# Performance work log

Measured on AMD Instinct MI355X. Metric: run time of the kernel, lower is better.

## Reference

```python
import jax, jax.numpy as jnp
import numpy as np


def setup_inputs() -> dict:
    key = jax.random.key(0)
    x = jax.random.normal(key, (256, 128, 2048), dtype=jnp.float32)
    return {"x": x}


def reference(x) -> jnp.ndarray:
    # x: (batch, channels, time)
    # 1) average reference: subtract mean across channels per (batch, time)
    x = x - jnp.mean(x, axis=1, keepdims=True)
    # 2) channel-wise zscore: mean/std over time axis per (batch, channel)
    mean = jnp.mean(x, axis=2, keepdims=True)
    std = jnp.std(x, axis=2, keepdims=True)  # population std (ddof=0), matches np.std
    std = jnp.where(std == 0, jnp.ones_like(std), std)
    return (x - mean) / std
```

## Files before the change

kernel.cpp:

```cpp
#include <hip/hip_runtime.h>


#define B 256
#define C 128
#define T 2048
#define T4 (T / 4)

typedef float f4 __attribute__((ext_vector_type(4)));

__launch_bounds__(1024)
__global__ void eeg_fused(const float* __restrict__ x, float* __restrict__ out) {
    const int b = blockIdx.x;
    const int tid = threadIdx.x;

    __shared__ float4 mu4[T4];
    __shared__ float4 part[T4];

    const float4* __restrict__ xb =
        reinterpret_cast<const float4*>(x) + (size_t)b * C * T4;
    float4* __restrict__ ob =
        reinterpret_cast<float4*>(out) + (size_t)b * C * T4;

    {
        const int t4 = tid & (T4 - 1);
        const int g  = tid >> 9;
        const float4* __restrict__ xp = xb + (size_t)(g * 64) * T4 + t4;

        float4 acc = make_float4(0.f, 0.f, 0.f, 0.f);
        #pragma unroll 8
        for (int k = 0; k < 64; ++k) {
            float4 v = xp[(size_t)k * T4];
            acc.x += v.x; acc.y += v.y; acc.z += v.z; acc.w += v.w;
        }
        if (g) part[t4] = acc;
        else   mu4[t4]  = acc;
        __syncthreads();
        if (!g) {
            const float invC = 1.0f / (float)C;
            float4 p = part[t4];
            float4 m = mu4[t4];
            m.x = (m.x + p.x) * invC;
            m.y = (m.y + p.y) * invC;
            m.z = (m.z + p.z) * invC;
            m.w = (m.w + p.w) * invC;
            mu4[t4] = m;
        }
        __syncthreads();
    }

    const int wave = tid >> 6;
    const int lane = tid & 63;
    const float invT = 1.0f / (float)T;

    for (int cc = wave; cc < C; cc += 16) {
        const int c = (C - 1) - cc;
        const float4* __restrict__ xc = xb + (size_t)c * T4;

        float4 y[8];
        float sum = 0.f, sq = 0.f;
        #pragma unroll
        for (int j = 0; j < 8; ++j) {
            float4 v = xc[lane + j * 64];
            float4 m = mu4[lane + j * 64];
            y[j].x = v.x - m.x; y[j].y = v.y - m.y;
            y[j].z = v.z - m.z; y[j].w = v.w - m.w;
            sum += (y[j].x + y[j].y) + (y[j].z + y[j].w);
            sq  += (y[j].x * y[j].x + y[j].y * y[j].y)
                 + (y[j].z * y[j].z + y[j].w * y[j].w);
        }

        #pragma unroll
        for (int off = 32; off > 0; off >>= 1) {
            sum += __shfl_xor(sum, off, 64);
            sq  += __shfl_xor(sq,  off, 64);
        }

        float mean = sum * invT;
        float var  = fmaxf(sq * invT - mean * mean, 0.f);
        float sd   = sqrtf(var);
        float inv  = (sd == 0.f) ? 1.0f : 1.0f / sd;

        float4* __restrict__ oc = ob + (size_t)c * T4;
        #pragma unroll
        for (int j = 0; j < 8; ++j) {
            f4 o = { (y[j].x - mean) * inv,
                     (y[j].y - mean) * inv,
                     (y[j].z - mean) * inv,
                     (y[j].w - mean) * inv };
            __builtin_nontemporal_store(
                o, reinterpret_cast<f4*>(oc + lane + j * 64));
        }
    }
}

extern "C" void kernel_launch(void* const* d_in, const int* in_sizes, int n_in,
                              void* d_out, int out_size, void* d_ws, size_t ws_size,
                              hipStream_t stream) {
    const float* x = (const float*)d_in[0];
    float* out = (float*)d_out;
    (void)d_ws; (void)ws_size;

    eeg_fused<<<B, 1024, 0, stream>>>(x, out);
}
```

Before: 465.8 us.

## Split fused kernel into channel-mean pass and per-row zscore kernel

Replaces the single per-batch 1024-thread kernel with two launches: one computing the channel mean per (batch,time) into workspace using many small blocks, and one where each wave z-scores a single (batch,channel) row. This raises parallelism far beyond one block per batch and removes the intra-block barrier phase. The cost is a second full read of the input from global memory plus a workspace round-trip and an extra launch.

```diff
diff --git a/kernel.cpp b/kernel.cpp
--- a/kernel.cpp
+++ b/kernel.cpp
@@ -8,88 +8,86 @@
 
 typedef float f4 __attribute__((ext_vector_type(4)));
 
-__launch_bounds__(1024)
-__global__ void eeg_fused(const float* __restrict__ x, float* __restrict__ out) {
-    const int b = blockIdx.x;
+__launch_bounds__(256)
+__global__ void mu_kernel(const float* __restrict__ x, float* __restrict__ mu) {
+    const int b = blockIdx.y;
+    const int t0 = blockIdx.x * 256;
     const int tid = threadIdx.x;
+    const int wave = tid >> 6;
+    const int lane = tid & 63;
 
-    __shared__ float4 mu4[T4];
-    __shared__ float4 part[T4];
+    const float4* __restrict__ xp =
+        reinterpret_cast<const float4*>(x + ((size_t)b * C + wave * 32) * T + t0);
 
-    const float4* __restrict__ xb =
-        reinterpret_cast<const float4*>(x) + (size_t)b * C * T4;
-    float4* __restrict__ ob =
-        reinterpret_cast<float4*>(out) + (size_t)b * C * T4;
-
-    {
-        const int t4 = tid & (T4 - 1);
-        const int g  = tid >> 9;
-        const float4* __restrict__ xp = xb + (size_t)(g * 64) * T4 + t4;
-
-        float4 acc = make_float4(0.f, 0.f, 0.f, 0.f);
-        #pragma unroll 8
-        for (int k = 0; k < 64; ++k) {
-            float4 v = xp[(size_t)k * T4];
-            acc.x += v.x; acc.y += v.y; acc.z += v.z; acc.w += v.w;
-        }
-        if (g) part[t4] = acc;
-        else   mu4[t4]  = acc;
-        __syncthreads();
-        if (!g) {
-            const float invC = 1.0f / (float)C;
-            float4 p = part[t4];
-            float4 m = mu4[t4];
-            m.x = (m.x + p.x) * invC;
-            m.y = (m.y + p.y) * invC;
-            m.z = (m.z + p.z) * invC;
-            m.w = (m.w + p.w) * invC;
-            mu4[t4] = m;
-        }
-        __syncthreads();
+    float4 acc = make_float4(0.f, 0.f, 0.f, 0.f);
+    #pragma unroll 8
+    for (int k = 0; k < 32; ++k) {
+        float4 v = xp[(size_t)k * T4 + lane];
+        acc.x += v.x; acc.y += v.y; acc.z += v.z; acc.w += v.w;
     }
 
-    const int wave = tid >> 6;
-    const int lane = tid & 63;
+    __shared__ float4 part[4][64];
+    part[wave][lane] = acc;
+    __syncthreads();
+
+    if (wave == 0) {
+        float4 p0 = part[0][lane], p1 = part[1][lane];
+        float4 p2 = part[2][lane], p3 = part[3][lane];
+        const float invC = 1.0f / (float)C;
+        float4 s;
+        s.x = (p0.x + p1.x + p2.x + p3.x) * invC;
+        s.y = (p0.y + p1.y + p2.y + p3.y) * invC;
+        s.z = (p0.z + p1.z + p2.z + p3.z) * invC;
+        s.w = (p0.w + p1.w + p2.w + p3.w) * invC;
+        reinterpret_cast<float4*>(mu + (size_t)b * T + t0)[lane] = s;
+    }
+}
+
+__launch_bounds__(256)
+__global__ void zscore_wave(const float* __restrict__ x,
+                            const float* __restrict__ mu,
+                            float* __restrict__ out) {
+    const int wave = threadIdx.x >> 6;
+    const int lane = threadIdx.x & 63;
+    const int bc = blockIdx.x * 4 + wave;
+    const int b = bc >> 7;
+
+    const float4* __restrict__ xc = reinterpret_cast<const float4*>(x) + (size_t)bc * T4;
+    const float4* __restrict__ mc = reinterpret_cast<const float4*>(mu) + (size_t)b * T4;
+
+    float4 y[8];
+    float sum = 0.f, sq = 0.f;
+    #pragma unroll
+    for (int j = 0; j < 8; ++j) {
+        float4 v = xc[lane + j * 64];
+        float4 m = mc[lane + j * 64];
+        y[j].x = v.x - m.x; y[j].y = v.y - m.y;
+        y[j].z = v.z - m.z; y[j].w = v.w - m.w;
+        sum += (y[j].x + y[j].y) + (y[j].z + y[j].w);
+        sq  += (y[j].x * y[j].x + y[j].y * y[j].y)
+             + (y[j].z * y[j].z + y[j].w * y[j].w);
+    }
+
+    #pragma unroll
+    for (int off = 32; off > 0; off >>= 1) {
+        sum += __shfl_xor(sum, off, 64);
+        sq  += __shfl_xor(sq,  off, 64);
+    }
+
     const float invT = 1.0f / (float)T;
+    float mean = sum * invT;
+    float var  = fmaxf(sq * invT - mean * mean, 0.f);
+    float sd   = sqrtf(var);
+    float inv  = (sd == 0.f) ? 1.0f : 1.0f / sd;
 
-    for (int cc = wave; cc < C; cc += 16) {
-        const int c = (C - 1) - cc;
-        const float4* __restrict__ xc = xb + (size_t)c * T4;
-
-        float4 y[8];
-        float sum = 0.f, sq = 0.f;
-        #pragma unroll
-        for (int j = 0; j < 8; ++j) {
-            float4 v = xc[lane + j * 64];
-            float4 m = mu4[lane + j * 64];
-            y[j].x = v.x - m.x; y[j].y = v.y - m.y;
-            y[j].z = v.z - m.z; y[j].w = v.w - m.w;
-            sum += (y[j].x + y[j].y) + (y[j].z + y[j].w);
-            sq  += (y[j].x * y[j].x + y[j].y * y[j].y)
-                 + (y[j].z * y[j].z + y[j].w * y[j].w);
-        }
-
-        #pragma unroll
-        for (int off = 32; off > 0; off >>= 1) {
-            sum += __shfl_xor(sum, off, 64);
-            sq  += __shfl_xor(sq,  off, 64);
-        }
-
-        float mean = sum * invT;
-        float var  = fmaxf(sq * invT - mean * mean, 0.f);
-        float sd   = sqrtf(var);
-        float inv  = (sd == 0.f) ? 1.0f : 1.0f / sd;
-
-        float4* __restrict__ oc = ob + (size_t)c * T4;
-        #pragma unroll
-        for (int j = 0; j < 8; ++j) {
-            f4 o = { (y[j].x - mean) * inv,
-                     (y[j].y - mean) * inv,
-                     (y[j].z - mean) * inv,
-                     (y[j].w - mean) * inv };
-            __builtin_nontemporal_store(
-                o, reinterpret_cast<f4*>(oc + lane + j * 64));
-        }
+    float4* __restrict__ oc = reinterpret_cast<float4*>(out) + (size_t)bc * T4;
+    #pragma unroll
+    for (int j = 0; j < 8; ++j) {
+        f4 o = { (y[j].x - mean) * inv,
+                 (y[j].y - mean) * inv,
+                 (y[j].z - mean) * inv,
+                 (y[j].w - mean) * inv };
+        __builtin_nontemporal_store(o, reinterpret_cast<f4*>(oc + lane + j * 64));
     }
 }
 
@@ -98,7 +96,9 @@
                               hipStream_t stream) {
     const float* x = (const float*)d_in[0];
     float* out = (float*)d_out;
-    (void)d_ws; (void)ws_size;
+    float* mu = (float*)d_ws;
 
-    eeg_fused<<<B, 1024, 0, stream>>>(x, out);
+    dim3 gridA(T / 256, B);
+    mu_kernel<<<gridA, 256, 0, stream>>>(x, mu);
+    zscore_wave<<<(B * C) / 4, 256, 0, stream>>>(x, mu, out);
 }
```

New measurement: 471.7 us. Within noise of the previous version (+1.3%).

## Keep a subset of channels in registers and LDS to avoid re-reading

Applied to the files above, without the earlier changes.

During the channel-mean pass, each thread now keeps 16 channel rows per group in registers and stashes 8 more per group in shared memory. Those 48 channels are normalized directly from on-chip copies, with cross-wave reductions for the register-held channels. Only the remaining 80 channels are re-read from global memory in the second pass, which cuts the extra read traffic. The cost is much higher register and LDS pressure, about 144KB of LDS per block, and extra barriers.

```diff
diff --git a/kernel.cpp b/kernel.cpp
--- a/kernel.cpp
+++ b/kernel.cpp
@@ -8,87 +8,166 @@
 
 typedef float f4 __attribute__((ext_vector_type(4)));
 
-__launch_bounds__(1024)
-__global__ void eeg_fused(const float* __restrict__ x, float* __restrict__ out) {
+__launch_bounds__(1024, 4)
+__global__ void eeg_fused3(const float* __restrict__ x, float* __restrict__ out) {
     const int b = blockIdx.x;
     const int tid = threadIdx.x;
+    const int t4 = tid & (T4 - 1);
+    const int g  = tid >> 9;
+    const int wave = tid >> 6;
+    const int lane = tid & 63;
 
     __shared__ float4 mu4[T4];
     __shared__ float4 part[T4];
+    __shared__ float4 stash[16][T4];
+    __shared__ float2 finals[32];
 
     const float4* __restrict__ xb =
         reinterpret_cast<const float4*>(x) + (size_t)b * C * T4;
     float4* __restrict__ ob =
         reinterpret_cast<float4*>(out) + (size_t)b * C * T4;
 
-    {
-        const int t4 = tid & (T4 - 1);
-        const int g  = tid >> 9;
-        const float4* __restrict__ xp = xb + (size_t)(g * 64) * T4 + t4;
+    const float4* __restrict__ xp = xb + (size_t)(g * 64) * T4 + t4;
+    float4 acc = make_float4(0.f, 0.f, 0.f, 0.f);
+    float4 v[16];
+    #pragma unroll
+    for (int k = 0; k < 16; ++k) {
+        v[k] = xp[(size_t)k * T4];
+        acc.x += v[k].x; acc.y += v[k].y; acc.z += v[k].z; acc.w += v[k].w;
+    }
+    #pragma unroll
+    for (int k = 16; k < 24; ++k) {
+        float4 w = xp[(size_t)k * T4];
+        stash[(g << 3) + (k - 16)][t4] = w;
+        acc.x += w.x; acc.y += w.y; acc.z += w.z; acc.w += w.w;
+    }
+    #pragma unroll 8
+    for (int k = 24; k < 64; ++k) {
+        float4 w = xp[(size_t)k * T4];
+        acc.x += w.x; acc.y += w.y; acc.z += w.z; acc.w += w.w;
+    }
+    if (g) part[t4] = acc;
+    else   mu4[t4]  = acc;
+    __syncthreads();
+    if (!g) {
+        const float invC = 1.0f / (float)C;
+        float4 p = part[t4], m0 = mu4[t4];
+        m0.x = (m0.x + p.x) * invC; m0.y = (m0.y + p.y) * invC;
+        m0.z = (m0.z + p.z) * invC; m0.w = (m0.w + p.w) * invC;
+        mu4[t4] = m0;
+    }
+    __syncthreads();
 
-        float4 acc = make_float4(0.f, 0.f, 0.f, 0.f);
-        #pragma unroll 8
-        for (int k = 0; k < 64; ++k) {
-            float4 v = xp[(size_t)k * T4];
-            acc.x += v.x; acc.y += v.y; acc.z += v.z; acc.w += v.w;
+    const float4 m = mu4[t4];
+    float2* comb = reinterpret_cast<float2*>(part);
+    #pragma unroll
+    for (int k = 0; k < 16; ++k) {
+        float yx = v[k].x - m.x, yy = v[k].y - m.y;
+        float yz = v[k].z - m.z, yw = v[k].w - m.w;
+        float s = (yx + yy) + (yz + yw);
+        float q = (yx * yx + yy * yy) + (yz * yz + yw * yw);
+        #pragma unroll
+        for (int off = 32; off > 0; off >>= 1) {
+            s += __shfl_xor(s, off, 64);
+            q += __shfl_xor(q, off, 64);
         }
-        if (g) part[t4] = acc;
-        else   mu4[t4]  = acc;
-        __syncthreads();
-        if (!g) {
-            const float invC = 1.0f / (float)C;
-            float4 p = part[t4];
-            float4 m = mu4[t4];
-            m.x = (m.x + p.x) * invC;
-            m.y = (m.y + p.y) * invC;
-            m.z = (m.z + p.z) * invC;
-            m.w = (m.w + p.w) * invC;
-            mu4[t4] = m;
+        if (lane == 0) comb[wave * 16 + k] = make_float2(s, q);
+    }
+    __syncthreads();
+    if (tid < 32) {
+        const int gg = tid >> 4, kk = tid & 15;
+        float s = 0.f, q = 0.f;
+        #pragma unroll
+        for (int w = 0; w < 8; ++w) {
+            float2 c2 = comb[(gg * 8 + w) * 16 + kk];
+            s += c2.x; q += c2.y;
         }
-        __syncthreads();
+        const float invT = 1.0f / (float)T;
+        float mean = s * invT;
+        float var  = fmaxf(q * invT - mean * mean, 0.f);
+        float sd   = sqrtf(var);
+        finals[tid] = make_float2(mean, (sd == 0.f) ? 1.0f : 1.0f / sd);
+    }
+    __syncthreads();
+    #pragma unroll
+    for (int k = 0; k < 16; ++k) {
+        float2 f = finals[g * 16 + k];
+        f4 o = { (v[k].x - m.x - f.x) * f.y,
+                 (v[k].y - m.y - f.x) * f.y,
+                 (v[k].z - m.z - f.x) * f.y,
+                 (v[k].w - m.w - f.x) * f.y };
+        __builtin_nontemporal_store(
+            o, reinterpret_cast<f4*>(ob + (size_t)(g * 64 + k) * T4 + t4));
     }
 
-    const int wave = tid >> 6;
-    const int lane = tid & 63;
+    {
+        const int si = wave;
+        const int ch = (si < 8) ? (16 + si) : (72 + si);
+        float4 yv[8];
+        float s = 0.f, q = 0.f;
+        #pragma unroll
+        for (int j = 0; j < 8; ++j) {
+            float4 vv = stash[si][lane + j * 64];
+            float4 mm = mu4[lane + j * 64];
+            yv[j].x = vv.x - mm.x; yv[j].y = vv.y - mm.y;
+            yv[j].z = vv.z - mm.z; yv[j].w = vv.w - mm.w;
+            s += (yv[j].x + yv[j].y) + (yv[j].z + yv[j].w);
+            q += (yv[j].x * yv[j].x + yv[j].y * yv[j].y)
+               + (yv[j].z * yv[j].z + yv[j].w * yv[j].w);
+        }
+        #pragma unroll
+        for (int off = 32; off > 0; off >>= 1) {
+            s += __shfl_xor(s, off, 64);
+            q += __shfl_xor(q, off, 64);
+        }
+        const float invT = 1.0f / (float)T;
+        float mean = s * invT;
+        float var  = fmaxf(q * invT - mean * mean, 0.f);
+        float sd   = sqrtf(var);
+        float inv  = (sd == 0.f) ? 1.0f : 1.0f / sd;
+        float4* __restrict__ oc = ob + (size_t)ch * T4;
+        #pragma unroll
+        for (int j = 0; j < 8; ++j) {
+            f4 o = { (yv[j].x - mean) * inv, (yv[j].y - mean) * inv,
+                     (yv[j].z - mean) * inv, (yv[j].w - mean) * inv };
+            __builtin_nontemporal_store(o, reinterpret_cast<f4*>(oc + lane + j * 64));
+        }
+    }
+
     const float invT = 1.0f / (float)T;
-
-    for (int cc = wave; cc < C; cc += 16) {
-        const int c = (C - 1) - cc;
+    for (int i = 0; i < 5; ++i) {
+        const int idx = i * 16 + wave;
+        const int c = (idx < 40) ? (127 - idx) : (103 - idx);
         const float4* __restrict__ xc = xb + (size_t)c * T4;
 
         float4 y[8];
-        float sum = 0.f, sq = 0.f;
+        float s = 0.f, q = 0.f;
         #pragma unroll
         for (int j = 0; j < 8; ++j) {
-            float4 v = xc[lane + j * 64];
-            float4 m = mu4[lane + j * 64];
-            y[j].x = v.x - m.x; y[j].y = v.y - m.y;
-            y[j].z = v.z - m.z; y[j].w = v.w - m.w;
-            sum += (y[j].x + y[j].y) + (y[j].z + y[j].w);
-            sq  += (y[j].x * y[j].x + y[j].y * y[j].y)
-                 + (y[j].z * y[j].z + y[j].w * y[j].w);
+            float4 vv = xc[lane + j * 64];
+            float4 mm = mu4[lane + j * 64];
+            y[j].x = vv.x - mm.x; y[j].y = vv.y - mm.y;
+            y[j].z = vv.z - mm.z; y[j].w = vv.w - mm.w;
+            s += (y[j].x + y[j].y) + (y[j].z + y[j].w);
+            q += (y[j].x * y[j].x + y[j].y * y[j].y)
+               + (y[j].z * y[j].z + y[j].w * y[j].w);
         }
-
         #pragma unroll
         for (int off = 32; off > 0; off >>= 1) {
-            sum += __shfl_xor(sum, off, 64);
-            sq  += __shfl_xor(sq,  off, 64);
+            s += __shfl_xor(s, off, 64);
+            q += __shfl_xor(q, off, 64);
         }
-
-        float mean = sum * invT;
-        float var  = fmaxf(sq * invT - mean * mean, 0.f);
+        float mean = s * invT;
+        float var  = fmaxf(q * invT - mean * mean, 0.f);
         float sd   = sqrtf(var);
         float inv  = (sd == 0.f) ? 1.0f : 1.0f / sd;
 
         float4* __restrict__ oc = ob + (size_t)c * T4;
         #pragma unroll
         for (int j = 0; j < 8; ++j) {
-            f4 o = { (y[j].x - mean) * inv,
-                     (y[j].y - mean) * inv,
-                     (y[j].z - mean) * inv,
-                     (y[j].w - mean) * inv };
-            __builtin_nontemporal_store(
-                o, reinterpret_cast<f4*>(oc + lane + j * 64));
+            f4 o = { (y[j].x - mean) * inv, (y[j].y - mean) * inv,
+                     (y[j].z - mean) * inv, (y[j].w - mean) * inv };
+            __builtin_nontemporal_store(o, reinterpret_cast<f4*>(oc + lane + j * 64));
         }
     }
 }
@@ -100,5 +179,5 @@
     float* out = (float*)d_out;
     (void)d_ws; (void)ws_size;
 
-    eeg_fused<<<B, 1024, 0, stream>>>(x, out);
+    eeg_fused3<<<B, 1024, 0, stream>>>(x, out);
 }
```

New measurement: 464.8 us. Within noise of the previous version (-0.2%).
